# Optimization experiments

Measured on AMD Instinct MI355X. Metric: run time of the kernel, lower is better.

## Reference

```python
import jax, jax.numpy as jnp
import numpy as np

L, D, B, N, E, T = 3, 64, 1024, 131072, 1048576, 16
CH, HID = L * D, (L * D) // 2  # channel_dim=192, reduction=2 -> 96
BN_EPS = 1e-5


def setup_inputs() -> dict:
    key = jax.random.key(0)
    ks = jax.random.split(key, 20)
    rn = lambda k, sh, s=0.1: jax.random.normal(k, sh, jnp.float32) * s
    return {
        "query_x": rn(ks[0], (N, D), 1.0),
        "corpus_x": rn(ks[1], (N, D), 1.0),
        "query_edge_index": jax.random.randint(ks[2], (2, E), 0, N),
        "corpus_edge_index": jax.random.randint(ks[3], (2, E), 0, N),
        "query_graph_idx": jnp.sort(jax.random.randint(ks[4], (N,), 0, B)),
        "corpus_graph_idx": jnp.sort(jax.random.randint(ks[5], (N,), 0, B)),
        "gin_w1": rn(ks[6], (L, D, D)),
        "gin_b1": jnp.zeros((L, D), jnp.float32),
        "gin_w2": rn(ks[7], (L, D, D)),
        "gin_b2": jnp.zeros((L, D), jnp.float32),
        "bn_gamma": jnp.ones((L, D), jnp.float32),
        "bn_beta": jnp.zeros((L, D), jnp.float32),
        "gin_eps": jnp.zeros((L,), jnp.float32),
        "inner_w": rn(ks[8], (L, D, D)),
        "inner_b": jnp.zeros((L, D), jnp.float32),
        "outer_w": rn(ks[9], (L, D, D)),
        "outer_b": jnp.zeros((L, D), jnp.float32),
        "conv_w1": rn(ks[10], (CH, HID)),
        "conv_b1": jnp.zeros((HID,), jnp.float32),
        "conv_w2": rn(ks[11], (HID, HID)),
        "conv_b2": jnp.zeros((HID,), jnp.float32),
        "score_w1": rn(ks[12], (HID, 16)),
        "score_b1": jnp.zeros((16,), jnp.float32),
        "score_w2": rn(ks[13], (16, 1)),
        "score_b2": jnp.zeros((1,), jnp.float32),
        "ntn_w": rn(ks[14], (D, D, T), 0.05),
        "ntn_wb": rn(ks[15], (T, 2 * D), 0.05),
        "ntn_bias": jnp.zeros((T,), jnp.float32),
        "sim_w1": rn(ks[16], (T, T)),
        "sim_b1": jnp.zeros((T,), jnp.float32),
        "sim_w2": rn(ks[17], (T, 1)),
        "sim_b2": jnp.zeros((1,), jnp.float32),
        "alpha": jnp.ones((1,), jnp.float32),
        "beta": jnp.ones((1,), jnp.float32),
    }


def _encode(x, edge_index, graph_idx, p):
    """EncodingLayer: per layer GINConv -> ReLU -> inner MLP -> segment-sum pool -> outer MLP."""
    src, dst = edge_index[0], edge_index[1]
    feats = []
    for i in range(L):
        agg = jax.ops.segment_sum(x[src], dst, num_segments=N)  # neighbor sum (gather->scatter)
        h = (1.0 + p["gin_eps"][i]) * x + agg                    # GIN aggregation
        h = jax.nn.relu(h @ p["gin_w1"][i] + p["gin_b1"][i]) @ p["gin_w2"][i] + p["gin_b2"][i]
        mu = h.mean(axis=0)
        var = h.var(axis=0)
        h = (h - mu) * jax.lax.rsqrt(var + BN_EPS) * p["bn_gamma"][i] + p["bn_beta"][i]  # BatchNorm1d (train stats)
        x = jax.nn.relu(h)
        inner = jax.nn.relu(x @ p["inner_w"][i] + p["inner_b"][i])
        pooled = jax.ops.segment_sum(inner, graph_idx, num_segments=B)  # [B, D] graph pooling
        feats.append(jax.nn.relu(pooled @ p["outer_w"][i] + p["outer_b"][i]))
    return jnp.concatenate(feats, axis=1)  # [B, L*D]


def reference(query_x, corpus_x, query_edge_index, corpus_edge_index, query_graph_idx, corpus_graph_idx, gin_w1, gin_b1, gin_w2, gin_b2, bn_gamma, bn_beta, gin_eps, inner_w, inner_b, outer_w, outer_b, conv_w1, conv_b1, conv_w2, conv_b2, score_w1, score_b1, score_w2, score_b2, ntn_w, ntn_wb, ntn_bias, sim_w1, sim_b1, sim_w2, sim_b2, alpha, beta):
    p = {"gin_w1": gin_w1, "gin_b1": gin_b1, "gin_w2": gin_w2, "gin_b2": gin_b2,
         "bn_gamma": bn_gamma, "bn_beta": bn_beta, "gin_eps": gin_eps,
         "inner_w": inner_w, "inner_b": inner_b, "outer_w": outer_w, "outer_b": outer_b}
    qf = _encode(query_x, query_edge_index, query_graph_idx, p)   # [B, CH]
    cf = _encode(corpus_x, corpus_edge_index, corpus_graph_idx, p)
    # diff branch: conv_stack + score_layer
    diff = jnp.exp(-jnp.square(qf - cf))
    h = jax.nn.relu(diff @ conv_w1 + conv_b1)
    h = jnp.tanh(h @ conv_w2 + conv_b2)
    score = jax.nn.sigmoid(jax.nn.relu(h @ score_w1 + score_b1) @ score_w2 + score_b2)[:, 0]
    # NTN interaction branch on last-layer (filters[-1]) graph embeddings
    e1, e2 = qf[:, -D:], cf[:, -D:]
    scoring = jnp.einsum('bf,fgt,bg->bt', e1, ntn_w, e2)
    block = jnp.concatenate([e1, e2], axis=1) @ ntn_wb.T
    sim_rep = jax.nn.relu(scoring + block + ntn_bias)
    sim = jax.nn.sigmoid(jax.nn.relu(sim_rep @ sim_w1 + sim_b1) @ sim_w2 + sim_b2)[:, 0]
    return alpha[0] * score + beta[0] * sim  # [B]
```

## Files before the change

### kernel.cpp

```cpp
#include <hip/hip_runtime.h>
#include <hip/hip_bf16.h>

typedef __hip_bfloat16 bf16;
typedef __attribute__((ext_vector_type(8))) short short8;
typedef __attribute__((ext_vector_type(4))) float floatx4;

#define NN     131072
#define NEDGE  1048576
#define BG     1024
#define LAYERS 3
#define TG     8

__device__ __forceinline__ short f2bf_s(float f){
    union { float f; unsigned u; } x; x.f = f;
    unsigned r = x.u + 0x7fffu + ((x.u >> 16) & 1u);
    return (short)(r >> 16);
}
__device__ __forceinline__ float bf2f_s(short s){
    union { unsigned u; float f; } x; x.u = ((unsigned)(unsigned short)s) << 16;
    return x.f;
}
__device__ __forceinline__ void acc4(const unsigned short* p,
                                     float& a0, float& a1, float& a2, float& a3){
    ushort4 u = *(const ushort4*)p;
    a0 += bf2f_s((short)u.x); a1 += bf2f_s((short)u.y);
    a2 += bf2f_s((short)u.z); a3 += bf2f_s((short)u.w);
}

__global__ __launch_bounds__(256) void k_zero(int* __restrict__ cnt,
    const float* __restrict__ pooled_prev, const float* __restrict__ owp,
    const float* __restrict__ obp, float* __restrict__ feats_prev)
{
    int i = blockIdx.x*256 + threadIdx.x;
    if (i < NN) cnt[i] = 0;
    if (pooled_prev && blockIdx.x < 256) {
        int bb = i >> 6, j = i & 63;
        const float* pr = pooled_prev + bb*64;
        float a = obp[j];
        for (int k = 0; k < 64; k++) a = fmaf(pr[k], owp[k*64 + j], a);
        feats_prev[bb*192 + 128 + j] = fmaxf(a, 0.f);
    }
}

__global__ __launch_bounds__(256) void k_hist(const int* __restrict__ ei,
                                              int* __restrict__ cnt,
                                              int* __restrict__ rank)
{
    int e = blockIdx.x*256 + threadIdx.x;
    rank[e] = atomicAdd(cnt + ei[NEDGE + e], 1);
}

__global__ __launch_bounds__(256) void k_scan1(const int* __restrict__ cnt,
    int* __restrict__ rowptr, int* __restrict__ bsum)
{
    __shared__ int sd[256];
    int t = threadIdx.x;
    int base = blockIdx.x*1024 + t*4;
    int c0 = cnt[base], c1 = cnt[base+1], c2 = cnt[base+2], c3 = cnt[base+3];
    int tsum = c0 + c1 + c2 + c3;
    sd[t] = tsum;
    __syncthreads();
    for (int off = 1; off < 256; off <<= 1) {
        int v = (t >= off) ? sd[t-off] : 0;
        __syncthreads();
        sd[t] += v;
        __syncthreads();
    }
    int excl = sd[t] - tsum;
    rowptr[base]   = excl;
    rowptr[base+1] = excl + c0;
    rowptr[base+2] = excl + c0 + c1;
    rowptr[base+3] = excl + c0 + c1 + c2;
    if (t == 255) bsum[blockIdx.x] = sd[255];
}

__global__ __launch_bounds__(128) void k_scan2(const int* __restrict__ bsum,
    int* __restrict__ boff, int* __restrict__ rowptr)
{
    __shared__ int sd[128];
    int t = threadIdx.x;
    int v0 = bsum[t];
    sd[t] = v0;
    __syncthreads();
    for (int off = 1; off < 128; off <<= 1) {
        int v = (t >= off) ? sd[t-off] : 0;
        __syncthreads();
        sd[t] += v;
        __syncthreads();
    }
    boff[t] = sd[t] - v0;
    if (t == 0) rowptr[NN] = NEDGE;
}

__global__ __launch_bounds__(256) void k_scan3(int* __restrict__ rowptr,
    const int* __restrict__ boff)
{
    int i = blockIdx.x*256 + threadIdx.x;
    rowptr[i] += boff[i >> 10];
}

__global__ __launch_bounds__(256) void k_fill(const int* __restrict__ ei,
    const int* __restrict__ rowptr, const int* __restrict__ rank,
    int* __restrict__ col)
{
    int e = blockIdx.x*256 + threadIdx.x;
    int s = ei[e];
    int d = ei[NEDGE + e];
    col[rowptr[d] + rank[e]] = s;
}

__global__ __launch_bounds__(256) void k_cvt(const float* __restrict__ x,
                                             bf16* __restrict__ xh,
                                             float* __restrict__ zbuf)
{
    int i = blockIdx.x*256 + threadIdx.x;
    float4 v = ((const float4*)x)[i];
    short4 o;
    o.x = f2bf_s(v.x); o.y = f2bf_s(v.y);
    o.z = f2bf_s(v.z); o.w = f2bf_s(v.w);
    ((short4*)xh)[i] = o;
    if (i < 3*128 + 3*BG*64) zbuf[i] = 0.f;
}

__global__ __launch_bounds__(256) void k_wprep(
    const float* __restrict__ gw1, const float* __restrict__ gw2,
    const float* __restrict__ iw,
    short* __restrict__ w1h, short* __restrict__ w1l,
    short* __restrict__ w2h, short* __restrict__ w2l,
    short* __restrict__ wih, short* __restrict__ wil)
{
    int i = blockIdx.x*256 + threadIdx.x;
    if (i >= 3*LAYERS*4096) return;
    int msel = i / (LAYERS*4096);
    int rem  = i % (LAYERS*4096);
    int l = rem >> 12, idx = rem & 4095;
    int n = idx >> 6, k = idx & 63;
    const float* src = (msel==0) ? gw1 : (msel==1) ? gw2 : iw;
    float v = src[l*4096 + k*64 + n];
    short hi = f2bf_s(v);
    short lo = f2bf_s(v - bf2f_s(hi));
    short* dh = (msel==0) ? w1h : (msel==1) ? w2h : wih;
    short* dl = (msel==0) ? w1l : (msel==1) ? w2l : wil;
    dh[rem] = hi;
    dl[rem] = lo;
}

__global__ __launch_bounds__(256) void k_agg_gin(
    const bf16* __restrict__ xh,
    const int* __restrict__ rowptr, const int* __restrict__ col,
    const float* __restrict__ epsp,
    const short* __restrict__ w1h, const short* __restrict__ w1l,
    const float* __restrict__ b1,
    const short* __restrict__ w2h, const short* __restrict__ w2l,
    const float* __restrict__ b2,
    unsigned short* __restrict__ bigh, float* __restrict__ stats,
    const float* __restrict__ pooled_prev, const float* __restrict__ owp,
    const float* __restrict__ obp, float* __restrict__ feats, int coffp)
{
    __shared__ __align__(16) char buf[4][9472];
    __shared__ float red[2][4][64];
    int tid = threadIdx.x, wv = tid >> 6, lane = tid & 63;
    int q = lane >> 4, m = lane & 15;
    int nb = blockIdx.x*128 + wv*32;
    short* Sh = (short*)buf[wv];
    short* Sl = Sh + 2304;
    float ep = 1.0f + *epsp;

    if (pooled_prev && blockIdx.x < 256) {
        int g = blockIdx.x*256 + tid;
        int bb = g >> 6, j = g & 63;
        const float* pr = pooled_prev + bb*64;
        float a = obp[j];
        for (int k = 0; k < 64; k++) a = fmaf(pr[k], owp[k*64 + j], a);
        feats[bb*192 + coffp + j] = fmaxf(a, 0.f);
    }

    int gv = rowptr[nb + (lane < 33 ? lane : 32)];
    int fo = m * 4;
    const unsigned short* xt = (const unsigned short*)xh;

    for (int i = 0; i < 8; i++) {
        int row = i*4 + q;
        int rs = __shfl(gv, row, 64);
        int re = __shfl(gv, row+1, 64);
        float a0=0.f,a1=0.f,a2=0.f,a3=0.f;
        float e0=0.f,e1=0.f,e2=0.f,e3=0.f;
        float g0=0.f,g1=0.f,g2=0.f,g3=0.f;
        float h0=0.f,h1=0.f,h2=0.f,h3=0.f;
        int r = rs;
        for (; r + 4 <= re; r += 4) {
            int ca = col[r], cb = col[r+1], cc = col[r+2], cd = col[r+3];
            acc4(xt + (((size_t)ca) << 6) + fo, a0,a1,a2,a3);
            acc4(xt + (((size_t)cb) << 6) + fo, e0,e1,e2,e3);
            acc4(xt + (((size_t)cc) << 6) + fo, g0,g1,g2,g3);
            acc4(xt + (((size_t)cd) << 6) + fo, h0,h1,h2,h3);
        }
        for (; r < re; r++)
            acc4(xt + (((size_t)col[r]) << 6) + fo, a0,a1,a2,a3);
        a0 += e0 + g0 + h0;
        a1 += e1 + g1 + h1;
        a2 += e2 + g2 + h2;
        a3 += e3 + g3 + h3;
        ushort4 sv = *(const ushort4*)(xt + (((size_t)(nb+row)) << 6) + fo);
        a0 = fmaf(ep, bf2f_s((short)sv.x), a0);
        a1 = fmaf(ep, bf2f_s((short)sv.y), a1);
        a2 = fmaf(ep, bf2f_s((short)sv.z), a2);
        a3 = fmaf(ep, bf2f_s((short)sv.w), a3);
        short4 hh, ll;
        hh.x = f2bf_s(a0); ll.x = f2bf_s(a0 - bf2f_s(hh.x));
        hh.y = f2bf_s(a1); ll.y = f2bf_s(a1 - bf2f_s(hh.y));
        hh.z = f2bf_s(a2); ll.z = f2bf_s(a2 - bf2f_s(hh.z));
        hh.w = f2bf_s(a3); ll.w = f2bf_s(a3 - bf2f_s(hh.w));
        *(short4*)(Sh + row*72 + fo) = hh;
        *(short4*)(Sl + row*72 + fo) = ll;
    }
    __syncthreads();

    short8 Ah[2][2], Al[2][2];
    #pragma unroll
    for (int mc=0; mc<2; mc++)
      #pragma unroll
      for (int kc=0; kc<2; kc++){
        Ah[mc][kc] = *(const short8*)(Sh + (mc*16+m)*72 + kc*32 + q*8);
        Al[mc][kc] = *(const short8*)(Sl + (mc*16+m)*72 + kc*32 + q*8);
      }
    floatx4 acc[2][4];
    #pragma unroll
    for (int mc=0;mc<2;mc++)
      #pragma unroll
      for (int nc=0;nc<4;nc++) acc[mc][nc] = (floatx4){0.f,0.f,0.f,0.f};
    #pragma unroll
    for (int nc=0;nc<4;nc++){
      #pragma unroll
      for (int kc=0;kc<2;kc++){
        short8 bh = *(const short8*)(w1h + (nc*16+m)*64 + kc*32 + q*8);
        short8 bl = *(const short8*)(w1l + (nc*16+m)*64 + kc*32 + q*8);
        #pragma unroll
        for (int mc=0;mc<2;mc++){
          acc[mc][nc] = __builtin_amdgcn_mfma_f32_16x16x32_bf16(Ah[mc][kc], bh, acc[mc][nc],0,0,0);
          acc[mc][nc] = __builtin_amdgcn_mfma_f32_16x16x32_bf16(Al[mc][kc], bh, acc[mc][nc],0,0,0);
          acc[mc][nc] = __builtin_amdgcn_mfma_f32_16x16x32_bf16(Ah[mc][kc], bl, acc[mc][nc],0,0,0);
        }
      }
    }

    #pragma unroll
    for (int nc=0;nc<4;nc++){
      float bia = b1[nc*16+m];
      #pragma unroll
      for (int mc=0;mc<2;mc++)
        #pragma unroll
        for (int r=0;r<4;r++){
          float v = fmaxf(acc[mc][nc][r] + bia, 0.f);
          int row = mc*16 + q*4 + r, cl = nc*16 + m;
          short hb = f2bf_s(v);
          Sh[row*72+cl] = hb;
          Sl[row*72+cl] = f2bf_s(v - bf2f_s(hb));
        }
    }
    __syncthreads();

    short8 A2h[2][2], A2l[2][2];
    #pragma unroll
    for (int mc=0; mc<2; mc++)
      #pragma unroll
      for (int kc=0; kc<2; kc++){
        A2h[mc][kc] = *(const short8*)(Sh + (mc*16+m)*72 + kc*32 + q*8);
        A2l[mc][kc] = *(const short8*)(Sl + (mc*16+m)*72 + kc*32 + q*8);
      }
    floatx4 acc2[2][4];
    #pragma unroll
    for (int mc=0;mc<2;mc++)
      #pragma unroll
      for (int nc=0;nc<4;nc++) acc2[mc][nc] = (floatx4){0.f,0.f,0.f,0.f};
    #pragma unroll
    for (int nc=0;nc<4;nc++){
      #pragma unroll
      for (int kc=0;kc<2;kc++){
        short8 bh = *(const short8*)(w2h + (nc*16+m)*64 + kc*32 + q*8);
        short8 bl = *(const short8*)(w2l + (nc*16+m)*64 + kc*32 + q*8);
        #pragma unroll
        for (int mc=0;mc<2;mc++){
          acc2[mc][nc] = __builtin_amdgcn_mfma_f32_16x16x32_bf16(A2h[mc][kc], bh, acc2[mc][nc],0,0,0);
          acc2[mc][nc] = __builtin_amdgcn_mfma_f32_16x16x32_bf16(A2l[mc][kc], bh, acc2[mc][nc],0,0,0);
          acc2[mc][nc] = __builtin_amdgcn_mfma_f32_16x16x32_bf16(A2h[mc][kc], bl, acc2[mc][nc],0,0,0);
        }
      }
    }

    #pragma unroll
    for (int nc=0;nc<4;nc++){
      float bia = b2[nc*16+m];
      float s = 0.f, s2 = 0.f;
      #pragma unroll
      for (int mc=0;mc<2;mc++)
        #pragma unroll
        for (int r=0;r<4;r++){
          float v = acc2[mc][nc][r] + bia;
          bigh[(((size_t)(nb + mc*16 + q*4 + r)) << 6) + nc*16 + m] =
              (unsigned short)f2bf_s(v);
          s += v; s2 = fmaf(v, v, s2);
        }
      s  += __shfl_xor(s, 16, 64);  s  += __shfl_xor(s, 32, 64);
      s2 += __shfl_xor(s2,16, 64);  s2 += __shfl_xor(s2,32, 64);
      if (q == 0){ red[0][wv][nc*16+m] = s; red[1][wv][nc*16+m] = s2; }
    }
    __syncthreads();
    if (tid < 128){
      int which = tid >> 6, c = tid & 63;
      float a = red[which][0][c]+red[which][1][c]+red[which][2][c]+red[which][3][c];
      unsafeAtomicAdd(stats + which*64 + c, a);
    }
}

__global__ __launch_bounds__(256) void k_bn_inner(
    const unsigned short* __restrict__ bigh, const float* __restrict__ stats,
    const float* __restrict__ gam, const float* __restrict__ bet,
    const short* __restrict__ wih, const short* __restrict__ wil,
    const float* __restrict__ bi,
    bf16* __restrict__ xh,
    const int* __restrict__ gidx, float* __restrict__ pooled)
{
    __shared__ __align__(16) char buf[4][9472];
    int tid = threadIdx.x, wv = tid >> 6, lane = tid & 63;
    int q = lane >> 4, m = lane & 15;
    int nb = blockIdx.x*128 + wv*32;
    short* Sh = (short*)buf[wv];
    short* Sl = Sh + 2304;

    float mu  = stats[lane]    * (1.0f/NN);
    float ex2 = stats[64+lane] * (1.0f/NN);
    float var = ex2 - mu*mu;
    float sc  = gam[lane] * rsqrtf(var + 1e-5f);
    float sh  = bet[lane] - mu*sc;

    for (int rr = 0; rr < 32; rr++){
        float v = bf2f_s((short)bigh[(((size_t)(nb+rr)) << 6) + lane]);
        v = fmaxf(fmaf(v, sc, sh), 0.f);
        xh[(((size_t)(nb+rr)) << 6) + lane] = __float2bfloat16(v);
        short hb = f2bf_s(v);
        Sh[rr*72 + lane] = hb;
        Sl[rr*72 + lane] = f2bf_s(v - bf2f_s(hb));
    }
    __syncthreads();

    short8 A2h[2][2], A2l[2][2];
    #pragma unroll
    for (int mc=0; mc<2; mc++)
      #pragma unroll
      for (int kc=0; kc<2; kc++){
        A2h[mc][kc] = *(const short8*)(Sh + (mc*16+m)*72 + kc*32 + q*8);
        A2l[mc][kc] = *(const short8*)(Sl + (mc*16+m)*72 + kc*32 + q*8);
      }
    floatx4 acc[2][4];
    #pragma unroll
    for (int mc=0;mc<2;mc++)
      #pragma unroll
      for (int nc=0;nc<4;nc++) acc[mc][nc] = (floatx4){0.f,0.f,0.f,0.f};
    #pragma unroll
    for (int nc=0;nc<4;nc++){
      #pragma unroll
      for (int kc=0;kc<2;kc++){
        short8 bh = *(const short8*)(wih + (nc*16+m)*64 + kc*32 + q*8);
        short8 bl = *(const short8*)(wil + (nc*16+m)*64 + kc*32 + q*8);
        #pragma unroll
        for (int mc=0;mc<2;mc++){
          acc[mc][nc] = __builtin_amdgcn_mfma_f32_16x16x32_bf16(A2h[mc][kc], bh, acc[mc][nc],0,0,0);
          acc[mc][nc] = __builtin_amdgcn_mfma_f32_16x16x32_bf16(A2l[mc][kc], bh, acc[mc][nc],0,0,0);
          acc[mc][nc] = __builtin_amdgcn_mfma_f32_16x16x32_bf16(A2h[mc][kc], bl, acc[mc][nc],0,0,0);
        }
      }
    }
    __syncthreads();

    float* P = (float*)buf[wv];
    #pragma unroll
    for (int nc=0;nc<4;nc++){
      float bia = bi[nc*16+m];
      #pragma unroll
      for (int mc=0;mc<2;mc++)
        #pragma unroll
        for (int r=0;r<4;r++){
          float v = fmaxf(acc[mc][nc][r] + bia, 0.f);
          P[(mc*16 + q*4 + r)*66 + nc*16 + m] = v;
        }
    }
    __syncthreads();

    int gv = (lane < 32) ? gidx[nb + lane] : 0;
    int cur = __shfl(gv, 0, 64);
    float a = 0.f;
    for (int rr = 0; rr < 32; rr++){
        int g = __shfl(gv, rr, 64);
        if (g != cur){
            unsafeAtomicAdd(pooled + (size_t)cur*64 + lane, a);
            a = 0.f; cur = g;
        }
        a += P[rr*66 + lane];
    }
    unsafeAtomicAdd(pooled + (size_t)cur*64 + lane, a);
}

__global__ __launch_bounds__(256) void k_tail(
    const float* __restrict__ qf, const float* __restrict__ cf,
    const float* __restrict__ pooled_c2,
    const float* __restrict__ ow2, const float* __restrict__ ob2,
    const float* __restrict__ cw1, const float* __restrict__ cb1,
    const float* __restrict__ cw2, const float* __restrict__ cb2,
    const float* __restrict__ sw1, const float* __restrict__ sb1,
    const float* __restrict__ sw2, const float* __restrict__ sb2,
    const float* __restrict__ nw,  const float* __restrict__ nwb,
    const float* __restrict__ nb,
    const float* __restrict__ mw1, const float* __restrict__ mb1,
    const float* __restrict__ mw2, const float* __restrict__ mb2,
    const float* __restrict__ alpha, const float* __restrict__ beta,
    float* __restrict__ out)
{
    __shared__ float cws[192*96];
    __shared__ float diff[TG][192];
    __shared__ float e1s[TG][64], e2s[TG][64];
    __shared__ float h1s[TG][96], h2s[TG][96];
    __shared__ float s1s[TG][16], s2s[TG][16], srep[TG][16];
    __shared__ float red[16][16][TG];

    int t = threadIdx.x;
    int b0 = blockIdx.x * TG;

    {
        int b = t >> 5, o = (t & 31) * 2;
        const float* pr = pooled_c2 + (size_t)(b0 + b)*64;
        float a0 = ob2[o], a1 = ob2[o+1];
        for (int k = 0; k < 64; k++) {
            float p = pr[k];
            a0 = fmaf(p, ow2[k*64 + o], a0);
            a1 = fmaf(p, ow2[k*64 + o + 1], a1);
        }
        e2s[b][o]   = fmaxf(a0, 0.f);
        e2s[b][o+1] = fmaxf(a1, 0.f);
    }
    for (int i = t; i < 192*96; i += 256) cws[i] = cw1[i];
    __syncthreads();

    for (int i = t; i < TG*192; i += 256) {
        int b = i / 192, f = i % 192;
        float qv = qf[(b0+b)*192 + f];
        float cv = (f < 128) ? cf[(b0+b)*192 + f] : e2s[b][f-128];
        float d = qv - cv;
        diff[b][f] = __expf(-d*d);
        if (f >= 128) e1s[b][f-128] = qv;
    }
    __syncthreads();

    {
        int b = t >> 5, o = (t & 31) * 3;
        float a0 = cb1[o], a1 = cb1[o+1], a2 = cb1[o+2];
        for (int f = 0; f < 192; f++) {
            float d = diff[b][f];
            const float* w = cws + f*96 + o;
            a0 = fmaf(d, w[0], a0);
            a1 = fmaf(d, w[1], a1);
            a2 = fmaf(d, w[2], a2);
        }
        h1s[b][o] = fmaxf(a0, 0.f);
        h1s[b][o+1] = fmaxf(a1, 0.f);
        h1s[b][o+2] = fmaxf(a2, 0.f);
    }
    __syncthreads();
    for (int i = t; i < 96*96; i += 256) cws[i] = cw2[i];
    __syncthreads();
    {
        int b = t >> 5, o = (t & 31) * 3;
        float a0 = cb2[o], a1 = cb2[o+1], a2 = cb2[o+2];
        for (int f = 0; f < 96; f++) {
            float d = h1s[b][f];
            const float* w = cws + f*96 + o;
            a0 = fmaf(d, w[0], a0);
            a1 = fmaf(d, w[1], a1);
            a2 = fmaf(d, w[2], a2);
        }
        h2s[b][o] = tanhf(a0);
        h2s[b][o+1] = tanhf(a1);
        h2s[b][o+2] = tanhf(a2);
    }
    __syncthreads();
    if (t < TG*16) {
        int b = t >> 4, o = t & 15;
        float a = sb1[o];
        for (int f = 0; f < 96; f++) a = fmaf(h2s[b][f], sw1[f*16+o], a);
        s1s[b][o] = fmaxf(a, 0.f);
    }

    {
        int tt = t & 15, gq = t >> 4;
        int g0 = gq * 4;
        int lane = t & 63;
        float e1v[TG];
        #pragma unroll
        for (int b = 0; b < TG; b++) e1v[b] = e1s[b][lane];
        float v0[TG], v1[TG], v2[TG], v3[TG];
        #pragma unroll
        for (int b = 0; b < TG; b++) { v0[b]=0.f; v1[b]=0.f; v2[b]=0.f; v3[b]=0.f; }
        for (int f = 0; f < 64; f++) {
            const float* wp = nw + ((size_t)f*64 + g0)*16 + tt;
            float w0 = wp[0], w1 = wp[16], w2 = wp[32], w3 = wp[48];
            #pragma unroll
            for (int b = 0; b < TG; b++) {
                float e = __shfl(e1v[b], f, 64);
                v0[b] = fmaf(e, w0, v0[b]);
                v1[b] = fmaf(e, w1, v1[b]);
                v2[b] = fmaf(e, w2, v2[b]);
                v3[b] = fmaf(e, w3, v3[b]);
            }
        }
        #pragma unroll
        for (int b = 0; b < TG; b++) {
            float p = v0[b]*e2s[b][g0] + v1[b]*e2s[b][g0+1]
                    + v2[b]*e2s[b][g0+2] + v3[b]*e2s[b][g0+3];
            red[gq][tt][b] = p;
        }
    }
    __syncthreads();
    if (t < TG*16) {
        int b = t >> 4, tt = t & 15;
        float scv = 0.f;
        #pragma unroll
        for (int gq = 0; gq < 16; gq++) scv += red[gq][tt][b];
        float blk = nb[tt];
        for (int f = 0; f < 64; f++) blk = fmaf(e1s[b][f], nwb[tt*128 + f], blk);
        for (int f = 0; f < 64; f++) blk = fmaf(e2s[b][f], nwb[tt*128 + 64 + f], blk);
        srep[b][tt] = fmaxf(scv + blk, 0.f);
    }
    __syncthreads();
    if (t < TG*16) {
        int b = t >> 4, o = t & 15;
        float a = mb1[o];
        #pragma unroll
        for (int f = 0; f < 16; f++) a = fmaf(srep[b][f], mw1[f*16+o], a);
        s2s[b][o] = fmaxf(a, 0.f);
    }
    __syncthreads();
    if (t < TG) {
        float sco = sb2[0], sm = mb2[0];
        #pragma unroll
        for (int f = 0; f < 16; f++) {
            sco = fmaf(s1s[t][f], sw2[f], sco);
            sm  = fmaf(s2s[t][f], mw2[f], sm);
        }
        float score = 1.f / (1.f + __expf(-sco));
        float sim   = 1.f / (1.f + __expf(-sm));
        out[b0 + t] = alpha[0]*score + beta[0]*sim;
    }
}

extern "C" void kernel_launch(void* const* d_in, const int* in_sizes, int n_in,
                              void* d_out, int out_size, void* d_ws, size_t ws_size,
                              hipStream_t stream)
{
    const float* qx  = (const float*)d_in[0];
    const float* cx  = (const float*)d_in[1];
    const int*   qei = (const int*)d_in[2];
    const int*   cei = (const int*)d_in[3];
    const int*   qgi = (const int*)d_in[4];
    const int*   cgi = (const int*)d_in[5];
    const float* Wgw1 = (const float*)d_in[6];
    const float* Wgb1 = (const float*)d_in[7];
    const float* Wgw2 = (const float*)d_in[8];
    const float* Wgb2 = (const float*)d_in[9];
    const float* Wgam = (const float*)d_in[10];
    const float* Wbet = (const float*)d_in[11];
    const float* Weps = (const float*)d_in[12];
    const float* Wiw  = (const float*)d_in[13];
    const float* Wib  = (const float*)d_in[14];
    const float* Wow  = (const float*)d_in[15];
    const float* Wob  = (const float*)d_in[16];
    const float* Wcw1 = (const float*)d_in[17];
    const float* Wcb1 = (const float*)d_in[18];
    const float* Wcw2 = (const float*)d_in[19];
    const float* Wcb2 = (const float*)d_in[20];
    const float* Wsw1 = (const float*)d_in[21];
    const float* Wsb1 = (const float*)d_in[22];
    const float* Wsw2 = (const float*)d_in[23];
    const float* Wsb2 = (const float*)d_in[24];
    const float* Wnw  = (const float*)d_in[25];
    const float* Wnwb = (const float*)d_in[26];
    const float* Wnb  = (const float*)d_in[27];
    const float* Wmw1 = (const float*)d_in[28];
    const float* Wmb1 = (const float*)d_in[29];
    const float* Wmw2 = (const float*)d_in[30];
    const float* Wmb2 = (const float*)d_in[31];
    const float* Wal  = (const float*)d_in[32];
    const float* Wbe  = (const float*)d_in[33];

    float* F      = (float*)d_ws;
    float* big    = F;
    float* zbuf   = F + 8388608;
    float* stats3 = zbuf;
    float* pooled3= zbuf + 384;
    float* qf     = pooled3 + 3*BG*64;
    float* cf     = qf + 196608;
    int*   rowptr = (int*)(cf + 196608);
    int*   cnt    = rowptr + (NN + 1);
    int*   col    = cnt + NN;
    int*   bsum   = col + NEDGE;
    int*   boff   = bsum + 128;
    bf16*  xh     = (bf16*)(boff + 128);
    int*   rank   = (int*)big;
    unsigned short* bigh = (unsigned short*)big;
    uintptr_t wtb = (uintptr_t)(xh + (size_t)NN*64);
    wtb = (wtb + 63) & ~((uintptr_t)63);
    short* w1h = (short*)wtb;
    short* w1l = w1h + 3*4096;
    short* w2h = w1l + 3*4096;
    short* w2l = w2h + 3*4096;
    short* wih = w2l + 3*4096;
    short* wil = wih + 3*4096;

    k_wprep<<<144, 256, 0, stream>>>(Wgw1, Wgw2, Wiw, w1h, w1l, w2h, w2l, wih, wil);

    for (int side = 0; side < 2; side++) {
        const float* x0 = side ? cx  : qx;
        const int* ei   = side ? cei : qei;
        const int* gi   = side ? cgi : qgi;
        float* feats    = side ? cf  : qf;

        if (side == 0)
            k_zero<<<NN/256, 256, 0, stream>>>(cnt, nullptr, nullptr, nullptr, nullptr);
        else
            k_zero<<<NN/256, 256, 0, stream>>>(cnt, pooled3 + 2*BG*64,
                                               Wow + 2*4096, Wob + 2*64, qf);
        k_hist<<<NEDGE/256, 256, 0, stream>>>(ei, cnt, rank);
        k_scan1<<<128, 256, 0, stream>>>(cnt, rowptr, bsum);
        k_scan2<<<1, 128, 0, stream>>>(bsum, boff, rowptr);
        k_scan3<<<NN/256, 256, 0, stream>>>(rowptr, boff);
        k_fill<<<NEDGE/256, 256, 0, stream>>>(ei, rowptr, rank, col);

        k_cvt<<<NN*64/1024, 256, 0, stream>>>(x0, xh, zbuf);

        for (int l = 0; l < LAYERS; l++) {
            const float* pprev = (l == 0) ? nullptr : pooled3 + (size_t)(l-1)*BG*64;
            const float* owp   = (l == 0) ? nullptr : Wow + (l-1)*4096;
            const float* obp   = (l == 0) ? nullptr : Wob + (l-1)*64;
            k_agg_gin<<<NN/128, 256, 0, stream>>>(xh, rowptr, col, Weps + l,
                                                  w1h + l*4096, w1l + l*4096, Wgb1 + l*64,
                                                  w2h + l*4096, w2l + l*4096, Wgb2 + l*64,
                                                  bigh, stats3 + l*128,
                                                  pprev, owp, obp, feats, (l-1)*64);
            k_bn_inner<<<NN/128, 256, 0, stream>>>(bigh, stats3 + l*128,
                                                   Wgam + l*64, Wbet + l*64,
                                                   wih + l*4096, wil + l*4096,
                                                   Wib + l*64, xh, gi,
                                                   pooled3 + (size_t)l*BG*64);
        }
    }

    k_tail<<<BG/TG, 256, 0, stream>>>(qf, cf, pooled3 + 2*BG*64,
                                      Wow + 2*4096, Wob + 2*64,
                                      Wcw1, Wcb1, Wcw2, Wcb2,
                                      Wsw1, Wsb1, Wsw2, Wsb2,
                                      Wnw, Wnwb, Wnb, Wmw1, Wmb1, Wmw2, Wmb2,
                                      Wal, Wbe, (float*)d_out);
}
```

Baseline: 908.4 us.

## Batch query and corpus graphs into merged launches and fuse inner MLP into next aggregation

Both query and corpus graphs are processed together in a single CSR build and merged kernels with doubled grids. This halves the number of launches and gives each kernel more parallelism. The inner-MLP and pooling step of layer l is moved into the layer l+1 aggregation kernel, reading the BN-applied activations that are already in xh. A lightweight elementwise BN-apply kernel replaces the heavy bn_inner for the first layers. The workspace grows to hold both sides, and the fused kernel carries more registers and extra syncs.

```diff
diff --git a/kernel.cpp b/kernel.cpp
--- a/kernel.cpp
+++ b/kernel.cpp
@@ -10,6 +10,7 @@
 #define BG     1024
 #define LAYERS 3
 #define TG     8
+#define ZTOTM  (768 + 6*BG*64)
 
 __device__ __forceinline__ short f2bf_s(float f){
     union { float f; unsigned u; } x; x.f = f;
@@ -25,101 +26,6 @@
     ushort4 u = *(const ushort4*)p;
     a0 += bf2f_s((short)u.x); a1 += bf2f_s((short)u.y);
     a2 += bf2f_s((short)u.z); a3 += bf2f_s((short)u.w);
-}
-
-__global__ __launch_bounds__(256) void k_zero(int* __restrict__ cnt,
-    const float* __restrict__ pooled_prev, const float* __restrict__ owp,
-    const float* __restrict__ obp, float* __restrict__ feats_prev)
-{
-    int i = blockIdx.x*256 + threadIdx.x;
-    if (i < NN) cnt[i] = 0;
-    if (pooled_prev && blockIdx.x < 256) {
-        int bb = i >> 6, j = i & 63;
-        const float* pr = pooled_prev + bb*64;
-        float a = obp[j];
-        for (int k = 0; k < 64; k++) a = fmaf(pr[k], owp[k*64 + j], a);
-        feats_prev[bb*192 + 128 + j] = fmaxf(a, 0.f);
-    }
-}
-
-__global__ __launch_bounds__(256) void k_hist(const int* __restrict__ ei,
-                                              int* __restrict__ cnt,
-                                              int* __restrict__ rank)
-{
-    int e = blockIdx.x*256 + threadIdx.x;
-    rank[e] = atomicAdd(cnt + ei[NEDGE + e], 1);
-}
-
-__global__ __launch_bounds__(256) void k_scan1(const int* __restrict__ cnt,
-    int* __restrict__ rowptr, int* __restrict__ bsum)
-{
-    __shared__ int sd[256];
-    int t = threadIdx.x;
-    int base = blockIdx.x*1024 + t*4;
-    int c0 = cnt[base], c1 = cnt[base+1], c2 = cnt[base+2], c3 = cnt[base+3];
-    int tsum = c0 + c1 + c2 + c3;
-    sd[t] = tsum;
-    __syncthreads();
-    for (int off = 1; off < 256; off <<= 1) {
-        int v = (t >= off) ? sd[t-off] : 0;
-        __syncthreads();
-        sd[t] += v;
-        __syncthreads();
-    }
-    int excl = sd[t] - tsum;
-    rowptr[base]   = excl;
-    rowptr[base+1] = excl + c0;
-    rowptr[base+2] = excl + c0 + c1;
-    rowptr[base+3] = excl + c0 + c1 + c2;
-    if (t == 255) bsum[blockIdx.x] = sd[255];
-}
-
-__global__ __launch_bounds__(128) void k_scan2(const int* __restrict__ bsum,
-    int* __restrict__ boff, int* __restrict__ rowptr)
-{
-    __shared__ int sd[128];
-    int t = threadIdx.x;
-    int v0 = bsum[t];
-    sd[t] = v0;
-    __syncthreads();
-    for (int off = 1; off < 128; off <<= 1) {
-        int v = (t >= off) ? sd[t-off] : 0;
-        __syncthreads();
-        sd[t] += v;
-        __syncthreads();
-    }
-    boff[t] = sd[t] - v0;
-    if (t == 0) rowptr[NN] = NEDGE;
-}
-
-__global__ __launch_bounds__(256) void k_scan3(int* __restrict__ rowptr,
-    const int* __restrict__ boff)
-{
-    int i = blockIdx.x*256 + threadIdx.x;
-    rowptr[i] += boff[i >> 10];
-}
-
-__global__ __launch_bounds__(256) void k_fill(const int* __restrict__ ei,
-    const int* __restrict__ rowptr, const int* __restrict__ rank,
-    int* __restrict__ col)
-{
-    int e = blockIdx.x*256 + threadIdx.x;
-    int s = ei[e];
-    int d = ei[NEDGE + e];
-    col[rowptr[d] + rank[e]] = s;
-}
-
-__global__ __launch_bounds__(256) void k_cvt(const float* __restrict__ x,
-                                             bf16* __restrict__ xh,
-                                             float* __restrict__ zbuf)
-{
-    int i = blockIdx.x*256 + threadIdx.x;
-    float4 v = ((const float4*)x)[i];
-    short4 o;
-    o.x = f2bf_s(v.x); o.y = f2bf_s(v.y);
-    o.z = f2bf_s(v.z); o.w = f2bf_s(v.w);
-    ((short4*)xh)[i] = o;
-    if (i < 3*128 + 3*BG*64) zbuf[i] = 0.f;
 }
 
 __global__ __launch_bounds__(256) void k_wprep(
@@ -145,7 +51,99 @@
     dl[rem] = lo;
 }
 
-__global__ __launch_bounds__(256) void k_agg_gin(
+__global__ __launch_bounds__(256) void k_cvtM(const float* __restrict__ qx,
+                                              const float* __restrict__ cx,
+                                              bf16* __restrict__ xh,
+                                              int* __restrict__ cnt,
+                                              float* __restrict__ zbuf)
+{
+    int i = blockIdx.x*256 + threadIdx.x;
+    float4 v = (i < NN*16) ? ((const float4*)qx)[i]
+                           : ((const float4*)cx)[i - NN*16];
+    short4 o;
+    o.x = f2bf_s(v.x); o.y = f2bf_s(v.y);
+    o.z = f2bf_s(v.z); o.w = f2bf_s(v.w);
+    ((short4*)xh)[i] = o;
+    if (i < 2*NN)   cnt[i]  = 0;
+    if (i < ZTOTM)  zbuf[i] = 0.f;
+}
+
+__global__ __launch_bounds__(256) void k_histM(const int* __restrict__ qei,
+                                               const int* __restrict__ cei,
+                                               int* __restrict__ cnt,
+                                               int* __restrict__ rank)
+{
+    int e = blockIdx.x*256 + threadIdx.x;
+    int side = e >> 20;
+    int el = e & (NEDGE-1);
+    const int* ei = side ? cei : qei;
+    rank[e] = atomicAdd(cnt + ei[NEDGE + el] + side*NN, 1);
+}
+
+__global__ __launch_bounds__(256) void k_scan1M(const int* __restrict__ cnt,
+    int* __restrict__ rowptr, int* __restrict__ bsum)
+{
+    __shared__ int sd[256];
+    int t = threadIdx.x;
+    int base = blockIdx.x*1024 + t*4;
+    int c0 = cnt[base], c1 = cnt[base+1], c2 = cnt[base+2], c3 = cnt[base+3];
+    int tsum = c0 + c1 + c2 + c3;
+    sd[t] = tsum;
+    __syncthreads();
+    for (int off = 1; off < 256; off <<= 1) {
+        int v = (t >= off) ? sd[t-off] : 0;
+        __syncthreads();
+        sd[t] += v;
+        __syncthreads();
+    }
+    int excl = sd[t] - tsum;
+    rowptr[base]   = excl;
+    rowptr[base+1] = excl + c0;
+    rowptr[base+2] = excl + c0 + c1;
+    rowptr[base+3] = excl + c0 + c1 + c2;
+    if (t == 255) bsum[blockIdx.x] = sd[255];
+}
+
+__global__ __launch_bounds__(256) void k_scan2M(const int* __restrict__ bsum,
+    int* __restrict__ boff, int* __restrict__ rowptr)
+{
+    __shared__ int sd[256];
+    int t = threadIdx.x;
+    int v0 = bsum[t];
+    sd[t] = v0;
+    __syncthreads();
+    for (int off = 1; off < 256; off <<= 1) {
+        int v = (t >= off) ? sd[t-off] : 0;
+        __syncthreads();
+        sd[t] += v;
+        __syncthreads();
+    }
+    boff[t] = sd[t] - v0;
+    if (t == 0) rowptr[2*NN] = 2*NEDGE;
+}
+
+__global__ __launch_bounds__(256) void k_scan3M(int* __restrict__ rowptr,
+    const int* __restrict__ boff)
+{
+    int i = blockIdx.x*256 + threadIdx.x;
+    rowptr[i] += boff[i >> 10];
+}
+
+__global__ __launch_bounds__(256) void k_fillM(const int* __restrict__ qei,
+    const int* __restrict__ cei,
+    const int* __restrict__ rowptr, const int* __restrict__ rank,
+    int* __restrict__ col)
+{
+    int e = blockIdx.x*256 + threadIdx.x;
+    int side = e >> 20;
+    int el = e & (NEDGE-1);
+    const int* ei = side ? cei : qei;
+    int s = ei[el] + side*NN;
+    int d = ei[NEDGE + el] + side*NN;
+    col[rowptr[d] + rank[e]] = s;
+}
+
+__global__ __launch_bounds__(256) void k_agg_ginM(
     const bf16* __restrict__ xh,
     const int* __restrict__ rowptr, const int* __restrict__ col,
     const float* __restrict__ epsp,
@@ -154,25 +152,31 @@
     const short* __restrict__ w2h, const short* __restrict__ w2l,
     const float* __restrict__ b2,
     unsigned short* __restrict__ bigh, float* __restrict__ stats,
-    const float* __restrict__ pooled_prev, const float* __restrict__ owp,
-    const float* __restrict__ obp, float* __restrict__ feats, int coffp)
+    const short* __restrict__ wihp, const short* __restrict__ wilp,
+    const float* __restrict__ bip,
+    const int* __restrict__ gidx_q, const int* __restrict__ gidx_c,
+    float* __restrict__ pool_q, float* __restrict__ pool_c)
 {
     __shared__ __align__(16) char buf[4][9472];
     __shared__ float red[2][4][64];
+    int bid = blockIdx.x;
+    int side = bid >> 10;
     int tid = threadIdx.x, wv = tid >> 6, lane = tid & 63;
     int q = lane >> 4, m = lane & 15;
-    int nb = blockIdx.x*128 + wv*32;
+    int nb = bid*128 + wv*32;
     short* Sh = (short*)buf[wv];
     short* Sl = Sh + 2304;
     float ep = 1.0f + *epsp;
-
-    if (pooled_prev && blockIdx.x < 256) {
-        int g = blockIdx.x*256 + tid;
-        int bb = g >> 6, j = g & 63;
-        const float* pr = pooled_prev + bb*64;
-        float a = obp[j];
-        for (int k = 0; k < 64; k++) a = fmaf(pr[k], owp[k*64 + j], a);
-        feats[bb*192 + coffp + j] = fmaxf(a, 0.f);
+    const short* xs = (const short*)xh;
+
+    short8 A3[2][2];
+    if (wihp) {
+        #pragma unroll
+        for (int mc=0; mc<2; mc++)
+          #pragma unroll
+          for (int kc=0; kc<2; kc++)
+            A3[mc][kc] = *(const short8*)(xs + (((size_t)(nb + mc*16 + m)) << 6)
+                                             + kc*32 + q*8);
     }
 
     int gv = rowptr[nb + (lane < 33 ? lane : 32)];
@@ -309,27 +313,139 @@
     if (tid < 128){
       int which = tid >> 6, c = tid & 63;
       float a = red[which][0][c]+red[which][1][c]+red[which][2][c]+red[which][3][c];
-      unsafeAtomicAdd(stats + which*64 + c, a);
-    }
-}
-
-__global__ __launch_bounds__(256) void k_bn_inner(
+      unsafeAtomicAdd(stats + side*128 + which*64 + c, a);
+    }
+
+    if (wihp) {
+        floatx4 acc3[2][4];
+        #pragma unroll
+        for (int mc=0;mc<2;mc++)
+          #pragma unroll
+          for (int nc=0;nc<4;nc++) acc3[mc][nc] = (floatx4){0.f,0.f,0.f,0.f};
+        #pragma unroll
+        for (int nc=0;nc<4;nc++){
+          #pragma unroll
+          for (int kc=0;kc<2;kc++){
+            short8 bh = *(const short8*)(wihp + (nc*16+m)*64 + kc*32 + q*8);
+            short8 bl = *(const short8*)(wilp + (nc*16+m)*64 + kc*32 + q*8);
+            #pragma unroll
+            for (int mc=0;mc<2;mc++){
+              acc3[mc][nc] = __builtin_amdgcn_mfma_f32_16x16x32_bf16(A3[mc][kc], bh, acc3[mc][nc],0,0,0);
+              acc3[mc][nc] = __builtin_amdgcn_mfma_f32_16x16x32_bf16(A3[mc][kc], bl, acc3[mc][nc],0,0,0);
+            }
+          }
+        }
+        __syncthreads();
+        float* P = (float*)buf[wv];
+        #pragma unroll
+        for (int nc=0;nc<4;nc++){
+          float bia = bip[nc*16+m];
+          #pragma unroll
+          for (int mc=0;mc<2;mc++)
+            #pragma unroll
+            for (int r=0;r<4;r++){
+              float v = fmaxf(acc3[mc][nc][r] + bia, 0.f);
+              P[(mc*16 + q*4 + r)*66 + nc*16 + m] = v;
+            }
+        }
+        __syncthreads();
+
+        const int* gidx = side ? gidx_c : gidx_q;
+        float* pooled   = side ? pool_c : pool_q;
+        int ln = nb - side*NN;
+        int gv2 = (lane < 32) ? gidx[ln + lane] : 0;
+        int cur = __shfl(gv2, 0, 64);
+        float a = 0.f;
+        for (int rr = 0; rr < 32; rr++){
+            int g = __shfl(gv2, rr, 64);
+            if (g != cur){
+                unsafeAtomicAdd(pooled + (size_t)cur*64 + lane, a);
+                a = 0.f; cur = g;
+            }
+            a += P[rr*66 + lane];
+        }
+        unsafeAtomicAdd(pooled + (size_t)cur*64 + lane, a);
+    }
+}
+
+__global__ __launch_bounds__(256) void k_bn_apply(
+    const unsigned short* __restrict__ bigh, const float* __restrict__ stats,
+    const float* __restrict__ gam, const float* __restrict__ bet,
+    bf16* __restrict__ xh,
+    const float* __restrict__ pprev_q, const float* __restrict__ pprev_c,
+    const float* __restrict__ owp, const float* __restrict__ obp,
+    float* __restrict__ qf, float* __restrict__ cf, int coffp)
+{
+    __shared__ float scs[128], shs[128];
+    int t = threadIdx.x;
+    if (t < 128) {
+        int side = t >> 6, c = t & 63;
+        const float* st = stats + side*128;
+        float mu  = st[c]    * (1.0f/NN);
+        float ex2 = st[64+c] * (1.0f/NN);
+        float var = ex2 - mu*mu;
+        float sc  = gam[c] * rsqrtf(var + 1e-5f);
+        scs[t] = sc;
+        shs[t] = bet[c] - mu*sc;
+    }
+    if (owp && blockIdx.x < 512) {
+        int side = blockIdx.x >> 8;
+        int g = (blockIdx.x & 255)*256 + t;
+        int bb = g >> 6, j = g & 63;
+        const float* pr = (side ? pprev_c : pprev_q) + (size_t)bb*64;
+        float a = obp[j];
+        for (int k = 0; k < 64; k++) a = fmaf(pr[k], owp[k*64 + j], a);
+        (side ? cf : qf)[bb*192 + coffp + j] = fmaxf(a, 0.f);
+    }
+    __syncthreads();
+
+    int i = blockIdx.x*256 + t;
+    ushort4 u = ((const ushort4*)bigh)[i];
+    int e = i << 2;
+    int base = ((e >> 6) >> 17)*64 + (e & 63);
+    short4 o;
+    float v0 = fmaxf(fmaf(bf2f_s((short)u.x), scs[base],   shs[base]),   0.f);
+    float v1 = fmaxf(fmaf(bf2f_s((short)u.y), scs[base+1], shs[base+1]), 0.f);
+    float v2 = fmaxf(fmaf(bf2f_s((short)u.z), scs[base+2], shs[base+2]), 0.f);
+    float v3 = fmaxf(fmaf(bf2f_s((short)u.w), scs[base+3], shs[base+3]), 0.f);
+    o.x = f2bf_s(v0); o.y = f2bf_s(v1); o.z = f2bf_s(v2); o.w = f2bf_s(v3);
+    ((short4*)xh)[i] = o;
+}
+
+__global__ __launch_bounds__(256) void k_bn_innerM(
     const unsigned short* __restrict__ bigh, const float* __restrict__ stats,
     const float* __restrict__ gam, const float* __restrict__ bet,
     const short* __restrict__ wih, const short* __restrict__ wil,
     const float* __restrict__ bi,
     bf16* __restrict__ xh,
-    const int* __restrict__ gidx, float* __restrict__ pooled)
+    const int* __restrict__ gidx_q, const int* __restrict__ gidx_c,
+    float* __restrict__ pooled_q, float* __restrict__ pooled_c,
+    const float* __restrict__ pprev_q, const float* __restrict__ pprev_c,
+    const float* __restrict__ owp, const float* __restrict__ obp,
+    float* __restrict__ qf, float* __restrict__ cf, int coffp)
 {
     __shared__ __align__(16) char buf[4][9472];
+    int bid = blockIdx.x;
+    int side = bid >> 10;
+    int lb = bid & 1023;
     int tid = threadIdx.x, wv = tid >> 6, lane = tid & 63;
     int q = lane >> 4, m = lane & 15;
-    int nb = blockIdx.x*128 + wv*32;
+    int nb = bid*128 + wv*32;
     short* Sh = (short*)buf[wv];
     short* Sl = Sh + 2304;
 
-    float mu  = stats[lane]    * (1.0f/NN);
-    float ex2 = stats[64+lane] * (1.0f/NN);
+    if (owp && lb < 256) {
+        int g = lb*256 + tid;
+        int bb = g >> 6, j = g & 63;
+        const float* pr = (side ? pprev_c : pprev_q) + (size_t)bb*64;
+        float a = obp[j];
+        for (int k = 0; k < 64; k++) a = fmaf(pr[k], owp[k*64 + j], a);
+        (side ? cf : qf)[bb*192 + coffp + j] = fmaxf(a, 0.f);
+    }
+
+    const float* st = stats + side*128;
+    float mu  = st[lane]    * (1.0f/NN);
+    float ex2 = st[64+lane] * (1.0f/NN);
     float var = ex2 - mu*mu;
     float sc  = gam[lane] * rsqrtf(var + 1e-5f);
     float sh  = bet[lane] - mu*sc;
@@ -387,7 +503,10 @@
     }
     __syncthreads();
 
-    int gv = (lane < 32) ? gidx[nb + lane] : 0;
+    const int* gidx = side ? gidx_c : gidx_q;
+    float* pooled   = side ? pooled_c : pooled_q;
+    int ln = nb - side*NN;
+    int gv = (lane < 32) ? gidx[ln + lane] : 0;
     int cur = __shfl(gv, 0, 64);
     float a = 0.f;
     for (int rr = 0; rr < 32; rr++){
@@ -401,9 +520,9 @@
     unsafeAtomicAdd(pooled + (size_t)cur*64 + lane, a);
 }
 
-__global__ __launch_bounds__(256) void k_tail(
+__global__ __launch_bounds__(256) void k_tailM(
     const float* __restrict__ qf, const float* __restrict__ cf,
-    const float* __restrict__ pooled_c2,
+    const float* __restrict__ pooled_q2, const float* __restrict__ pooled_c2,
     const float* __restrict__ ow2, const float* __restrict__ ob2,
     const float* __restrict__ cw1, const float* __restrict__ cb1,
     const float* __restrict__ cw2, const float* __restrict__ cb2,
@@ -428,26 +547,30 @@
 
     {
         int b = t >> 5, o = (t & 31) * 2;
-        const float* pr = pooled_c2 + (size_t)(b0 + b)*64;
-        float a0 = ob2[o], a1 = ob2[o+1];
+        const float* prq = pooled_q2 + (size_t)(b0 + b)*64;
+        const float* prc = pooled_c2 + (size_t)(b0 + b)*64;
+        float q0 = ob2[o], q1 = ob2[o+1];
+        float c0 = ob2[o], c1 = ob2[o+1];
         for (int k = 0; k < 64; k++) {
-            float p = pr[k];
-            a0 = fmaf(p, ow2[k*64 + o], a0);
-            a1 = fmaf(p, ow2[k*64 + o + 1], a1);
-        }
-        e2s[b][o]   = fmaxf(a0, 0.f);
-        e2s[b][o+1] = fmaxf(a1, 0.f);
+            float w0 = ow2[k*64 + o], w1 = ow2[k*64 + o + 1];
+            float pq = prq[k], pc = prc[k];
+            q0 = fmaf(pq, w0, q0); q1 = fmaf(pq, w1, q1);
+            c0 = fmaf(pc, w0, c0); c1 = fmaf(pc, w1, c1);
+        }
+        e1s[b][o]   = fmaxf(q0, 0.f);
+        e1s[b][o+1] = fmaxf(q1, 0.f);
+        e2s[b][o]   = fmaxf(c0, 0.f);
+        e2s[b][o+1] = fmaxf(c1, 0.f);
     }
     for (int i = t; i < 192*96; i += 256) cws[i] = cw1[i];
     __syncthreads();
 
     for (int i = t; i < TG*192; i += 256) {
         int b = i / 192, f = i % 192;
-        float qv = qf[(b0+b)*192 + f];
+        float qv = (f < 128) ? qf[(b0+b)*192 + f] : e1s[b][f-128];
         float cv = (f < 128) ? cf[(b0+b)*192 + f] : e2s[b][f-128];
         float d = qv - cv;
         diff[b][f] = __expf(-d*d);
-        if (f >= 128) e1s[b][f-128] = qv;
     }
     __syncthreads();
 
@@ -591,22 +714,21 @@
     const float* Wal  = (const float*)d_in[32];
     const float* Wbe  = (const float*)d_in[33];
 
-    float* F      = (float*)d_ws;
-    float* big    = F;
-    float* zbuf   = F + 8388608;
+    float* F = (float*)d_ws;
+    unsigned short* bigh = (unsigned short*)F;
+    int*   rank   = (int*)F;
+    bf16*  xh     = (bf16*)(F + 8388608);
+    float* zbuf   = F + 16777216;
     float* stats3 = zbuf;
-    float* pooled3= zbuf + 384;
-    float* qf     = pooled3 + 3*BG*64;
+    float* pooled3= zbuf + 768;
+    float* qf     = F + 16777216 + ZTOTM;
     float* cf     = qf + 196608;
     int*   rowptr = (int*)(cf + 196608);
-    int*   cnt    = rowptr + (NN + 1);
-    int*   col    = cnt + NN;
-    int*   bsum   = col + NEDGE;
-    int*   boff   = bsum + 128;
-    bf16*  xh     = (bf16*)(boff + 128);
-    int*   rank   = (int*)big;
-    unsigned short* bigh = (unsigned short*)big;
-    uintptr_t wtb = (uintptr_t)(xh + (size_t)NN*64);
+    int*   cnt    = rowptr + (2*NN + 1);
+    int*   col    = cnt + 2*NN;
+    int*   bsum   = col + 2*NEDGE;
+    int*   boff   = bsum + 256;
+    uintptr_t wtb = (uintptr_t)(boff + 256);
     wtb = (wtb + 63) & ~((uintptr_t)63);
     short* w1h = (short*)wtb;
     short* w1l = w1h + 3*4096;
@@ -616,47 +738,54 @@
     short* wil = wih + 3*4096;
 
     k_wprep<<<144, 256, 0, stream>>>(Wgw1, Wgw2, Wiw, w1h, w1l, w2h, w2l, wih, wil);
-
-    for (int side = 0; side < 2; side++) {
-        const float* x0 = side ? cx  : qx;
-        const int* ei   = side ? cei : qei;
-        const int* gi   = side ? cgi : qgi;
-        float* feats    = side ? cf  : qf;
-
-        if (side == 0)
-            k_zero<<<NN/256, 256, 0, stream>>>(cnt, nullptr, nullptr, nullptr, nullptr);
-        else
-            k_zero<<<NN/256, 256, 0, stream>>>(cnt, pooled3 + 2*BG*64,
-                                               Wow + 2*4096, Wob + 2*64, qf);
-        k_hist<<<NEDGE/256, 256, 0, stream>>>(ei, cnt, rank);
-        k_scan1<<<128, 256, 0, stream>>>(cnt, rowptr, bsum);
-        k_scan2<<<1, 128, 0, stream>>>(bsum, boff, rowptr);
-        k_scan3<<<NN/256, 256, 0, stream>>>(rowptr, boff);
-        k_fill<<<NEDGE/256, 256, 0, stream>>>(ei, rowptr, rank, col);
-
-        k_cvt<<<NN*64/1024, 256, 0, stream>>>(x0, xh, zbuf);
-
-        for (int l = 0; l < LAYERS; l++) {
-            const float* pprev = (l == 0) ? nullptr : pooled3 + (size_t)(l-1)*BG*64;
-            const float* owp   = (l == 0) ? nullptr : Wow + (l-1)*4096;
-            const float* obp   = (l == 0) ? nullptr : Wob + (l-1)*64;
-            k_agg_gin<<<NN/128, 256, 0, stream>>>(xh, rowptr, col, Weps + l,
-                                                  w1h + l*4096, w1l + l*4096, Wgb1 + l*64,
-                                                  w2h + l*4096, w2l + l*4096, Wgb2 + l*64,
-                                                  bigh, stats3 + l*128,
-                                                  pprev, owp, obp, feats, (l-1)*64);
-            k_bn_inner<<<NN/128, 256, 0, stream>>>(bigh, stats3 + l*128,
-                                                   Wgam + l*64, Wbet + l*64,
-                                                   wih + l*4096, wil + l*4096,
-                                                   Wib + l*64, xh, gi,
-                                                   pooled3 + (size_t)l*BG*64);
-        }
-    }
-
-    k_tail<<<BG/TG, 256, 0, stream>>>(qf, cf, pooled3 + 2*BG*64,
-                                      Wow + 2*4096, Wob + 2*64,
-                                      Wcw1, Wcb1, Wcw2, Wcb2,
-                                      Wsw1, Wsb1, Wsw2, Wsb2,
-                                      Wnw, Wnwb, Wnb, Wmw1, Wmb1, Wmw2, Wmb2,
-                                      Wal, Wbe, (float*)d_out);
-}
+    k_cvtM  <<<16384, 256, 0, stream>>>(qx, cx, xh, cnt, zbuf);
+    k_histM <<<8192, 256, 0, stream>>>(qei, cei, cnt, rank);
+    k_scan1M<<<256, 256, 0, stream>>>(cnt, rowptr, bsum);
+    k_scan2M<<<1, 256, 0, stream>>>(bsum, boff, rowptr);
+    k_scan3M<<<1024, 256, 0, stream>>>(rowptr, boff);
+    k_fillM <<<8192, 256, 0, stream>>>(qei, cei, rowptr, rank, col);
+
+    float* pq0 = pooled3;
+    float* pc0 = pooled3 + (size_t)3*BG*64;
+    float* pq1 = pooled3 + (size_t)1*BG*64;
+    float* pc1 = pooled3 + (size_t)4*BG*64;
+    float* pq2 = pooled3 + (size_t)2*BG*64;
+    float* pc2 = pooled3 + (size_t)5*BG*64;
+
+    k_agg_ginM<<<2048, 256, 0, stream>>>(xh, rowptr, col, Weps + 0,
+                                         w1h, w1l, Wgb1, w2h, w2l, Wgb2,
+                                         bigh, stats3 + 0,
+                                         nullptr, nullptr, nullptr,
+                                         qgi, cgi, nullptr, nullptr);
+    k_bn_apply<<<16384, 256, 0, stream>>>(bigh, stats3 + 0, Wgam, Wbet, xh,
+                                          nullptr, nullptr, nullptr, nullptr,
+                                          qf, cf, 0);
+    k_agg_ginM<<<2048, 256, 0, stream>>>(xh, rowptr, col, Weps + 1,
+                                         w1h + 4096, w1l + 4096, Wgb1 + 64,
+                                         w2h + 4096, w2l + 4096, Wgb2 + 64,
+                                         bigh, stats3 + 256,
+                                         wih, wil, Wib,
+                                         qgi, cgi, pq0, pc0);
+    k_bn_apply<<<16384, 256, 0, stream>>>(bigh, stats3 + 256, Wgam + 64, Wbet + 64, xh,
+                                          pq0, pc0, Wow, Wob,
+                                          qf, cf, 0);
+    k_agg_ginM<<<2048, 256, 0, stream>>>(xh, rowptr, col, Weps + 2,
+                                         w1h + 2*4096, w1l + 2*4096, Wgb1 + 128,
+                                         w2h + 2*4096, w2l + 2*4096, Wgb2 + 128,
+                                         bigh, stats3 + 512,
+                                         wih + 4096, wil + 4096, Wib + 64,
+                                         qgi, cgi, pq1, pc1);
+    k_bn_innerM<<<2048, 256, 0, stream>>>(bigh, stats3 + 512,
+                                          Wgam + 128, Wbet + 128,
+                                          wih + 2*4096, wil + 2*4096, Wib + 128,
+                                          xh, qgi, cgi, pq2, pc2,
+                                          pq1, pc1, Wow + 4096, Wob + 64,
+                                          qf, cf, 64);
+
+    k_tailM<<<BG/TG, 256, 0, stream>>>(qf, cf, pq2, pc2,
+                                       Wow + 2*4096, Wob + 2*64,
+                                       Wcw1, Wcb1, Wcw2, Wcb2,
+                                       Wsw1, Wsb1, Wsw2, Wsb2,
+                                       Wnw, Wnwb, Wnb, Wmw1, Wmb1, Wmw2, Wmb2,
+                                       Wal, Wbe, (float*)d_out);
+}
```

After: 820.5 us, median of 2. 9.7% less time.
